# Performance work log

Measured on AMD Instinct MI355X. Metric: run time of the kernel, lower is better.

The kernel has to match this reference:

```python
import jax, jax.numpy as jnp
import numpy as np

IMG = 1024
P0, P1 = 32, 16          # patch_size = [32, 16], P0 = 2*P1 required by stride-2 conv
C = 1                    # num_channels (must be 1 for unflatten(encoded, 1) to be valid)
N0 = (IMG // P0) ** 2    # 1024 patches at coarse scale
N1 = (IMG // P1) ** 2    # 4096 patches at fine scale
D0 = C * P0 * P0         # 1024 projection dim (coarse)
D1 = C * P1 * P1         # 256 projection dim (fine)
B = 8
BN_EPS = 1e-3            # keras BatchNormalization default
LRELU_ALPHA = 0.3        # keras LeakyReLU default


def setup_inputs() -> dict:
    key = jax.random.key(0)
    ks = jax.random.split(key, 9)
    return {
        "X": jax.random.normal(ks[0], (B, IMG, IMG, C), jnp.float32),
        "W_emb": jax.random.normal(ks[1], (N0, D0), jnp.float32) * 0.02,
        "conv_w": jax.random.normal(ks[2], (3, 3, N0, N1), jnp.float32) * 0.02,
        "conv_b": jnp.zeros((N1,), jnp.float32),
        "bn_gamma": jax.random.uniform(ks[3], (N1,), jnp.float32) + 0.5,
        "bn_beta": jax.random.normal(ks[4], (N1,), jnp.float32) * 0.1,
        "bn_mean": jax.random.normal(ks[5], (N1,), jnp.float32) * 0.1,
        "bn_var": jax.random.uniform(ks[6], (N1,), jnp.float32) + 0.5,
        "W_dense": jax.random.normal(ks[7], (D0, D0), jnp.float32) * 0.02,
        "b_dense": jnp.zeros((D0,), jnp.float32),
    }


def _patches(x, p):
    # [B,H,W,C] -> [B, (H/p)*(W/p), p, p, C]; row-major patch order, matching tf split/stack path.
    b, h, w, c = x.shape
    x = x.reshape(b, h // p, p, w // p, p, c).transpose(0, 1, 3, 2, 4, 5)
    return x.reshape(b, (h // p) * (w // p), p, p, c)


def _unpatch(x):
    # [B, n, p, p, C] -> [B, e*p, e*p, C] with e = sqrt(n); exact inverse of _patches.
    b, n, p, _, c = x.shape
    e = int(np.sqrt(n))
    x = x.reshape(b, e, e, p, p, c).transpose(0, 1, 3, 2, 4, 5)
    return x.reshape(b, e * p, e * p, c)


def reference(X, W_emb, conv_w, conv_b, bn_gamma, bn_beta, bn_mean, bn_var, W_dense, b_dense):
    b = X.shape[0]
    # fine-scale patches, flattened
    flat = _patches(X, P1).reshape(b, N1, D1)

    # positional embedding 1: positions = arange(N0) -> full embedding table
    pos1 = W_emb  # [N0, D0]

    # positional embedding 2: unflatten -> conv branch (inference: dropout = identity, BN uses moving stats)
    pe = pos1.reshape(1, N0, P0, P0, C).transpose(0, 4, 2, 3, 1).reshape(C, P0, P0, N0)  # [C,P0,P0,N0]
    y = jax.lax.conv_general_dilated(
        pe, conv_w, window_strides=(2, 2), padding='SAME',
        dimension_numbers=('NHWC', 'HWIO', 'NHWC')) + conv_b            # [C, P1, P1, N1]
    y = (y - bn_mean) * (bn_gamma / jnp.sqrt(bn_var + BN_EPS)) + bn_beta
    y = jnp.where(y > 0, y, LRELU_ALPHA * y)
    pos2 = y.reshape(1, C, P1, P1, N1).transpose(0, 4, 2, 3, 1).reshape(1, N1, D1)

    enc = flat + pos2                                                    # [B, N1, D1]
    # unflatten(.,1) -> unpatch -> repatch at coarse scale (pure reshape/transpose)
    img = _unpatch(enc.reshape(b, N1, P1, P1, 1))                        # [B, IMG, IMG, 1]
    enc = _patches(img, P0).reshape(b, N0, D0) + pos1                    # [B, N0, D0]
    return enc @ W_dense + b_dense
```

## Files before the change

kernel.cpp:

```cpp
#include <hip/hip_runtime.h>

typedef __attribute__((ext_vector_type(8))) short short8;
typedef __attribute__((ext_vector_type(4))) short short4v;
typedef __attribute__((ext_vector_type(4))) float float4v;

typedef const void __attribute__((address_space(1)))* gptr_t;
typedef void __attribute__((address_space(3)))* lptr_t;

__device__ __forceinline__ void gload_lds16(const void* g, void* l) {
    __builtin_amdgcn_global_load_lds((gptr_t)g, (lptr_t)l, 16, 0, 0);
}

__device__ __forceinline__ unsigned short f2bf(float f) {
    union { float f; unsigned int u; } v; v.f = f;
    unsigned int r = v.u + 0x7fffu + ((v.u >> 16) & 1u);
    return (unsigned short)(r >> 16);
}

__device__ __forceinline__ short8 frag_ld(const unsigned char* base, int row, int k2) {
    return *(const short8*)(base + row * 128 + (k2 ^ ((row & 7) << 4)));
}

__device__ __forceinline__ int swzB(int n) {
    return ((n ^ (n >> 3)) & 7) << 4;
}

__device__ __forceinline__ short8 frag_ldB(const unsigned char* base, int n, int k2) {
    return *(const short8*)(base + n * 128 + (k2 ^ swzB(n)));
}

__device__ __forceinline__ float4v mfma_bf16(short8 a, short8 b, float4v c) {
    return __builtin_amdgcn_mfma_f32_16x16x32_bf16(a, b, c, 0, 0, 0);
}

__global__ __launch_bounds__(256) void k_transpose_bf16(
        const float* __restrict__ in, unsigned short* __restrict__ out,
        float* __restrict__ zb) {
    __shared__ float tile[32][33];
    int tx = threadIdx.x, ty = threadIdx.y;
    if (blockIdx.x == 0 && blockIdx.y == 0 && ty == 0) zb[tx] = 0.0f;
    int x = blockIdx.x * 32 + tx;
    int ybase = blockIdx.y * 32;
#pragma unroll
    for (int j = 0; j < 4; j++)
        tile[ty + j * 8][tx] = in[(size_t)(ybase + ty + j * 8) * 1024 + x];
    __syncthreads();
    int ox = ybase + tx;
    int oybase = blockIdx.x * 32;
#pragma unroll
    for (int j = 0; j < 4; j++)
        out[(size_t)(oybase + ty + j * 8) * 1024 + ox] = f2bf(tile[tx][ty + j * 8]);
}

__global__ __launch_bounds__(256, 3) void k_conv_gemm(
        const float* __restrict__ convw,
        const unsigned short* __restrict__ peT,
        const unsigned short* __restrict__ zerobuf,
        float* __restrict__ y_part)
{
    __shared__ __align__(16) unsigned char ldsA[2][16384];
    __shared__ __align__(16) unsigned char ldsB[2][8192];

    const int t = threadIdx.x;
    const int L = blockIdx.x;
    const int ell = (L & 7) * 144 + (L >> 3);
    const int mt = ell & 1;
    const int nt = (ell >> 1) & 63;
    const int s  = ell >> 7;
    const int kh = s / 3, kw = s - kh * 3;
    const int ncol0 = nt * 64;

    const int l = t & 63, w = t >> 6;
    const int wm = w >> 1, wn = w & 1;
    const int l15 = l & 15;
    const int lk2 = (l >> 4) * 16;

    float4v acc[4][2] = {};

    const unsigned short* asrc[4];
    int aok[4];
#pragma unroll
    for (int i = 0; i < 4; i++) {
        int idx = i * 256 + t;
        int r = idx >> 3, c8 = idx & 7;
        int m = mt * 128 + r;
        int oh = m >> 4, ow = m & 15;
        int ih = 2 * oh + kh, iw = 2 * ow + kw;
        bool ok = (ih < 32) && (iw < 32);
        asrc[i] = ok ? (peT + (size_t)(ih * 32 + iw) * 1024 + ((c8 ^ (r & 7)) * 8))
                     : zerobuf;
        aok[i] = ok ? ~0 : 0;
    }

    const int g = t >> 4, l16v = t & 15;
    const int bk0 = g * 4;
    const int bn0 = l16v * 4;
    const float* bbase = convw + ((size_t)s * 1024 + bk0) * 4096 + ncol0 + bn0;

    float4v rb[3][4];

#pragma unroll
    for (int i = 0; i < 4; i++)
        gload_lds16(asrc[i], &ldsA[0][(i * 256 + t) * 16]);
#pragma unroll
    for (int i = 0; i < 4; i++)
        rb[0][i] = *(const float4v*)(bbase + (size_t)i * 4096);
    __builtin_amdgcn_sched_barrier(0);
#pragma unroll
    for (int i = 0; i < 4; i++)
        gload_lds16(asrc[i] + (64 & aok[i]), &ldsA[1][(i * 256 + t) * 16]);
#pragma unroll
    for (int i = 0; i < 4; i++)
        rb[1][i] = *(const float4v*)(bbase + (size_t)(64 + i) * 4096);
    __builtin_amdgcn_sched_barrier(0);
#pragma unroll
    for (int i = 0; i < 4; i++)
        rb[2][i] = *(const float4v*)(bbase + (size_t)(128 + i) * 4096);
    asm volatile("s_waitcnt vmcnt(16)" ::: "memory");
    __builtin_amdgcn_sched_barrier(0);
#pragma unroll
    for (int i = 0; i < 4; i++) {
        int n = bn0 + i;
        short4v v;
        v.x = (short)f2bf(rb[0][0][i]);
        v.y = (short)f2bf(rb[0][1][i]);
        v.z = (short)f2bf(rb[0][2][i]);
        v.w = (short)f2bf(rb[0][3][i]);
        *(short4v*)(&ldsB[0][n * 128 + ((bk0 * 2) ^ swzB(n))]) = v;
    }
    asm volatile("s_waitcnt lgkmcnt(0)" ::: "memory");
    __builtin_amdgcn_s_barrier();

#pragma unroll
    for (int tt = 0; tt < 16; ++tt) {
        const int cur = tt & 1;

        short8 af[4][2], bfr[2][2];
#pragma unroll
        for (int mf = 0; mf < 4; mf++)
#pragma unroll
            for (int ks = 0; ks < 2; ks++)
                af[mf][ks] = frag_ld(ldsA[cur], wm * 64 + mf * 16 + l15, ks * 64 + lk2);
#pragma unroll
        for (int nf = 0; nf < 2; nf++)
#pragma unroll
            for (int ks = 0; ks < 2; ks++)
                bfr[nf][ks] = frag_ldB(ldsB[cur], wn * 32 + nf * 16 + l15, ks * 64 + lk2);
        asm volatile("s_waitcnt lgkmcnt(0)" ::: "memory");
        __builtin_amdgcn_sched_barrier(0);
        __builtin_amdgcn_s_barrier();
        __builtin_amdgcn_sched_barrier(0);

        if (tt < 14) {
            const int k0n = (tt + 2) * 64;
#pragma unroll
            for (int i = 0; i < 4; i++)
                gload_lds16(asrc[i] + (k0n & aok[i]), &ldsA[cur][(i * 256 + t) * 16]);
        }
        if (tt < 13) {
            const int k0b = (tt + 3) * 64;
#pragma unroll
            for (int i = 0; i < 4; i++)
                rb[tt % 3][i] = *(const float4v*)(bbase + (size_t)(k0b + i) * 4096);
        }

        __builtin_amdgcn_s_setprio(1);
#pragma unroll
        for (int mf = 0; mf < 4; mf++)
#pragma unroll
            for (int nf = 0; nf < 2; nf++)
#pragma unroll
                for (int ks = 0; ks < 2; ks++)
                    acc[mf][nf] = mfma_bf16(af[mf][ks], bfr[nf][ks], acc[mf][nf]);
        __builtin_amdgcn_s_setprio(0);

        if (tt < 15) {
            if (tt <= 12)      asm volatile("s_waitcnt vmcnt(16)" ::: "memory");
            else if (tt == 13) asm volatile("s_waitcnt vmcnt(12)" ::: "memory");
            else               asm volatile("s_waitcnt vmcnt(0)" ::: "memory");
            __builtin_amdgcn_sched_barrier(0);
#pragma unroll
            for (int i = 0; i < 4; i++) {
                int n = bn0 + i;
                short4v v;
                v.x = (short)f2bf(rb[(tt + 1) % 3][0][i]);
                v.y = (short)f2bf(rb[(tt + 1) % 3][1][i]);
                v.z = (short)f2bf(rb[(tt + 1) % 3][2][i]);
                v.w = (short)f2bf(rb[(tt + 1) % 3][3][i]);
                *(short4v*)(&ldsB[cur ^ 1][n * 128 + ((bk0 * 2) ^ swzB(n))]) = v;
            }
            asm volatile("s_waitcnt lgkmcnt(0)" ::: "memory");
            __builtin_amdgcn_sched_barrier(0);
            __builtin_amdgcn_s_barrier();
        }
    }

    float* yp = y_part + (size_t)s * 1048576;
#pragma unroll
    for (int mf = 0; mf < 4; mf++) {
        int row = mt * 128 + wm * 64 + mf * 16 + (l >> 4) * 4;
#pragma unroll
        for (int nf = 0; nf < 2; nf++) {
            int col = ncol0 + wn * 32 + nf * 16 + l15;
#pragma unroll
            for (int rr = 0; rr < 4; rr++)
                yp[(size_t)(row + rr) * 4096 + col] = acc[mf][nf][rr];
        }
    }
}

__global__ __launch_bounds__(256) void k_bn_pos2(
        const float* __restrict__ y_part, const float* __restrict__ cb,
        const float* __restrict__ gamma, const float* __restrict__ beta,
        const float* __restrict__ mean, const float* __restrict__ var,
        float* __restrict__ pos2img) {
    int idx = blockIdx.x * 256 + threadIdx.x;
    int m = idx >> 12, oc = idx & 4095;
    float v = cb[oc];
#pragma unroll
    for (int s = 0; s < 9; s++)
        v += y_part[(size_t)s * 1048576 + idx];
    v = (v - mean[oc]) * (gamma[oc] * rsqrtf(var[oc] + 1e-3f)) + beta[oc];
    v = v > 0.0f ? v : 0.3f * v;
    int y = ((oc >> 6) << 4) + (m >> 4);
    int x = ((oc & 63) << 4) + (m & 15);
    pos2img[y * 1024 + x] = v;
}

__global__ __launch_bounds__(256) void k_build_A(
        const float* __restrict__ X, const float* __restrict__ pos2img,
        const float* __restrict__ W_emb, unsigned short* __restrict__ Aenc) {
    int row = blockIdx.x;
    int n0 = row & 1023;
    int b  = row >> 10;
    int d0 = threadIdx.x * 4;
    int y = ((n0 >> 5) << 5) + (d0 >> 5);
    int x = ((n0 & 31) << 5) + (d0 & 31);
    size_t pix = (size_t)y * 1024 + x;
    float4v xv = *(const float4v*)(X + (size_t)b * 1048576 + pix);
    float4v pv = *(const float4v*)(pos2img + pix);
    float4v wv = *(const float4v*)(W_emb + (size_t)n0 * 1024 + d0);
    short4v o;
    o.x = (short)f2bf(xv.x + pv.x + wv.x);
    o.y = (short)f2bf(xv.y + pv.y + wv.y);
    o.z = (short)f2bf(xv.z + pv.z + wv.z);
    o.w = (short)f2bf(xv.w + pv.w + wv.w);
    *(short4v*)(Aenc + (size_t)row * 1024 + d0) = o;
}

__global__ __launch_bounds__(256) void k_final_gemm(
        const unsigned short* __restrict__ A,
        const unsigned short* __restrict__ Bt,
        const float* __restrict__ bias,
        float* __restrict__ C) {
    __shared__ __align__(16) unsigned char ldsA[16384];
    __shared__ __align__(16) unsigned char ldsB[16384];
    const int t = threadIdx.x;
    const int L = blockIdx.x;
    const int ell = (L & 7) * 64 + (L >> 3);
    const int col0 = (ell & 7) * 128;
    const int row0 = (ell >> 3) * 128;
    const int l = t & 63, w = t >> 6;
    const int wm = w >> 1, wn = w & 1;
    const int l15 = l & 15;
    const int lk2 = (l >> 4) * 16;

    float4v acc[4][4] = {};

    const unsigned short* asrc[4];
    const unsigned short* bsrc[4];
#pragma unroll
    for (int i = 0; i < 4; i++) {
        int idx = i * 256 + t;
        int r = idx >> 3, c8 = idx & 7;
        int cofs = (c8 ^ (r & 7)) * 8;
        asrc[i] = A  + (size_t)(row0 + r) * 1024 + cofs;
        bsrc[i] = Bt + (size_t)(col0 + r) * 1024 + cofs;
    }

    for (int k0 = 0; k0 < 1024; k0 += 64) {
#pragma unroll
        for (int i = 0; i < 4; i++) {
            int idx = i * 256 + t;
            gload_lds16(asrc[i] + k0, ldsA + idx * 16);
            gload_lds16(bsrc[i] + k0, ldsB + idx * 16);
        }
        __syncthreads();

        short8 af[4][2], bfr[4][2];
#pragma unroll
        for (int mf = 0; mf < 4; mf++)
#pragma unroll
            for (int ks = 0; ks < 2; ks++)
                af[mf][ks] = frag_ld(ldsA, wm * 64 + mf * 16 + l15, ks * 64 + lk2);
#pragma unroll
        for (int nf = 0; nf < 4; nf++)
#pragma unroll
            for (int ks = 0; ks < 2; ks++)
                bfr[nf][ks] = frag_ld(ldsB, wn * 64 + nf * 16 + l15, ks * 64 + lk2);
#pragma unroll
        for (int mf = 0; mf < 4; mf++)
#pragma unroll
            for (int nf = 0; nf < 4; nf++)
#pragma unroll
                for (int ks = 0; ks < 2; ks++)
                    acc[mf][nf] = mfma_bf16(af[mf][ks], bfr[nf][ks], acc[mf][nf]);
        __syncthreads();
    }

#pragma unroll
    for (int nf = 0; nf < 4; nf++) {
        int col = col0 + wn * 64 + nf * 16 + l15;
        float bv = bias[col];
#pragma unroll
        for (int mf = 0; mf < 4; mf++) {
            int row = row0 + wm * 64 + mf * 16 + (l >> 4) * 4;
#pragma unroll
            for (int r = 0; r < 4; r++)
                C[(size_t)(row + r) * 1024 + col] = acc[mf][nf][r] + bv;
        }
    }
}

extern "C" void kernel_launch(void* const* d_in, const int* in_sizes, int n_in,
                              void* d_out, int out_size, void* d_ws, size_t ws_size,
                              hipStream_t stream) {
    (void)in_sizes; (void)n_in; (void)out_size; (void)ws_size;
    const float* X       = (const float*)d_in[0];
    const float* W_emb   = (const float*)d_in[1];
    const float* conv_w  = (const float*)d_in[2];
    const float* conv_b  = (const float*)d_in[3];
    const float* gamma   = (const float*)d_in[4];
    const float* beta    = (const float*)d_in[5];
    const float* mean    = (const float*)d_in[6];
    const float* var     = (const float*)d_in[7];
    const float* W_dense = (const float*)d_in[8];
    const float* b_dense = (const float*)d_in[9];
    float* out = (float*)d_out;

    unsigned char* ws = (unsigned char*)d_ws;
    float*          y_part  = (float*)(ws);
    float*          zerobuf = (float*)(ws + (36u << 20));
    unsigned short* peT     = (unsigned short*)(ws + (38u << 20));
    unsigned short* WdT     = (unsigned short*)(ws + (40u << 20));
    float*          pos2img = (float*)(ws + (42u << 20));
    unsigned short* Aenc    = (unsigned short*)(ws + (48u << 20));

    dim3 tb(32, 8);
    k_transpose_bf16<<<dim3(32, 32), tb, 0, stream>>>(W_emb, peT, zerobuf);
    k_transpose_bf16<<<dim3(32, 32), tb, 0, stream>>>(W_dense, WdT, zerobuf);
    k_conv_gemm<<<1152, 256, 0, stream>>>(conv_w, peT, (const unsigned short*)zerobuf, y_part);
    k_bn_pos2<<<4096, 256, 0, stream>>>(y_part, conv_b, gamma, beta, mean, var, pos2img);
    k_build_A<<<8192, 256, 0, stream>>>(X, pos2img, W_emb, Aenc);
    k_final_gemm<<<512, 256, 0, stream>>>(Aenc, WdT, b_dense, out);
}
```

Baseline: 122.4 us.

## Remap conv GEMM output columns to strided runs and shorten weight prefetch depth

Each block's 64 output channels now come as four 16-wide runs spaced 512 channels apart instead of one contiguous 64-channel slab. The apparent aim is to spread concurrent blocks' weight reads across different memory channels and address ranges. The fp32 weight register prefetch drops from three stages to two, with the vmcnt waits adjusted to match, and the occupancy hint of 3 is removed from the launch bounds. The shallower prefetch frees registers but exposes more global-load latency per K step.

```diff
diff --git a/kernel.cpp b/kernel.cpp
--- a/kernel.cpp
+++ b/kernel.cpp
@@ -52,7 +52,7 @@
         out[(size_t)(oybase + ty + j * 8) * 1024 + ox] = f2bf(tile[tx][ty + j * 8]);
 }
 
-__global__ __launch_bounds__(256, 3) void k_conv_gemm(
+__global__ __launch_bounds__(256) void k_conv_gemm(
         const float* __restrict__ convw,
         const unsigned short* __restrict__ peT,
         const unsigned short* __restrict__ zerobuf,
@@ -68,7 +68,7 @@
     const int nt = (ell >> 1) & 63;
     const int s  = ell >> 7;
     const int kh = s / 3, kw = s - kh * 3;
-    const int ncol0 = nt * 64;
+    const int qbase = (nt < 32) ? nt : 96 + nt;
 
     const int l = t & 63, w = t >> 6;
     const int wm = w >> 1, wn = w & 1;
@@ -95,9 +95,10 @@
     const int g = t >> 4, l16v = t & 15;
     const int bk0 = g * 4;
     const int bn0 = l16v * 4;
-    const float* bbase = convw + ((size_t)s * 1024 + bk0) * 4096 + ncol0 + bn0;
-
-    float4v rb[3][4];
+    const int coln = (qbase + 32 * (l16v >> 2)) * 16 + (l16v & 3) * 4;
+    const float* bbase = convw + ((size_t)s * 1024 + bk0) * 4096 + coln;
+
+    float4v rb[2][4];
 
 #pragma unroll
     for (int i = 0; i < 4; i++)
@@ -112,11 +113,7 @@
 #pragma unroll
     for (int i = 0; i < 4; i++)
         rb[1][i] = *(const float4v*)(bbase + (size_t)(64 + i) * 4096);
-    __builtin_amdgcn_sched_barrier(0);
-#pragma unroll
-    for (int i = 0; i < 4; i++)
-        rb[2][i] = *(const float4v*)(bbase + (size_t)(128 + i) * 4096);
-    asm volatile("s_waitcnt vmcnt(16)" ::: "memory");
+    asm volatile("s_waitcnt vmcnt(8)" ::: "memory");
     __builtin_amdgcn_sched_barrier(0);
 #pragma unroll
     for (int i = 0; i < 4; i++) {
@@ -156,12 +153,9 @@
 #pragma unroll
             for (int i = 0; i < 4; i++)
                 gload_lds16(asrc[i] + (k0n & aok[i]), &ldsA[cur][(i * 256 + t) * 16]);
-        }
-        if (tt < 13) {
-            const int k0b = (tt + 3) * 64;
 #pragma unroll
             for (int i = 0; i < 4; i++)
-                rb[tt % 3][i] = *(const float4v*)(bbase + (size_t)(k0b + i) * 4096);
+                rb[cur][i] = *(const float4v*)(bbase + (size_t)(k0n + i) * 4096);
         }
 
         __builtin_amdgcn_s_setprio(1);
@@ -175,18 +169,17 @@
         __builtin_amdgcn_s_setprio(0);
 
         if (tt < 15) {
-            if (tt <= 12)      asm volatile("s_waitcnt vmcnt(16)" ::: "memory");
-            else if (tt == 13) asm volatile("s_waitcnt vmcnt(12)" ::: "memory");
-            else               asm volatile("s_waitcnt vmcnt(0)" ::: "memory");
+            if (tt < 14) asm volatile("s_waitcnt vmcnt(8)" ::: "memory");
+            else         asm volatile("s_waitcnt vmcnt(0)" ::: "memory");
             __builtin_amdgcn_sched_barrier(0);
 #pragma unroll
             for (int i = 0; i < 4; i++) {
                 int n = bn0 + i;
                 short4v v;
-                v.x = (short)f2bf(rb[(tt + 1) % 3][0][i]);
-                v.y = (short)f2bf(rb[(tt + 1) % 3][1][i]);
-                v.z = (short)f2bf(rb[(tt + 1) % 3][2][i]);
-                v.w = (short)f2bf(rb[(tt + 1) % 3][3][i]);
+                v.x = (short)f2bf(rb[cur ^ 1][0][i]);
+                v.y = (short)f2bf(rb[cur ^ 1][1][i]);
+                v.z = (short)f2bf(rb[cur ^ 1][2][i]);
+                v.w = (short)f2bf(rb[cur ^ 1][3][i]);
                 *(short4v*)(&ldsB[cur ^ 1][n * 128 + ((bk0 * 2) ^ swzB(n))]) = v;
             }
             asm volatile("s_waitcnt lgkmcnt(0)" ::: "memory");
@@ -201,7 +194,8 @@
         int row = mt * 128 + wm * 64 + mf * 16 + (l >> 4) * 4;
 #pragma unroll
         for (int nf = 0; nf < 2; nf++) {
-            int col = ncol0 + wn * 32 + nf * 16 + l15;
+            int run = wn * 2 + nf;
+            int col = (qbase + 32 * run) * 16 + l15;
 #pragma unroll
             for (int rr = 0; rr < 4; rr++)
                 yp[(size_t)(row + rr) * 4096 + col] = acc[mf][nf][rr];
```

New measurement: 117.5 us. 4.0% less time.
